# Kernel optimization log

Hardware: AMD Instinct MI355X
Metric: run time of the kernel (lower is better)

## Reference

```python
import jax, jax.numpy as jnp
import numpy as np
from jax import lax

B, T, D_IN, H, L = 512, 256, 2, 100, 3
G = 4 * H  # pytorch gate order: i, f, g, o


def _lstm_layer(xs, W_ih, W_hh, b):
    # xs: [T, B, Din]; W_ih: [4H, Din]; W_hh: [4H, H]; b: [4H] (b_ih + b_hh)
    pre = jnp.einsum('tbd,gd->tbg', xs, W_ih) + b  # [T, B, 4H]

    def step(carry, p):
        h, c = carry
        g = p + h @ W_hh.T
        i, f, gg, o = jnp.split(g, 4, axis=-1)
        c = jax.nn.sigmoid(f) * c + jax.nn.sigmoid(i) * jnp.tanh(gg)
        h = jax.nn.sigmoid(o) * jnp.tanh(c)
        return (h, c), h

    z = jnp.zeros((xs.shape[1], W_hh.shape[1]), xs.dtype)
    _, hs = lax.scan(step, (z, z), pre)
    return hs  # [T, B, H]


def setup_inputs() -> dict:
    key = jax.random.key(0)
    ks = jax.random.split(key, 8)
    s = 1.0 / np.sqrt(H)
    u = lambda k, shp: jax.random.uniform(k, shp, jnp.float32, -s, s)
    return {
        'x': jax.random.normal(ks[0], (B, T, D_IN), jnp.float32),
        'W_ih0': u(ks[1], (G, D_IN)),
        'W_ih_rest': u(ks[2], (L - 1, G, H)),
        'W_hh': u(ks[3], (L, G, H)),
        'b_ih': u(ks[4], (L, G)),
        'b_hh': u(ks[5], (L, G)),
        'head_w': u(ks[6], (1, H)),
        'head_b': u(ks[7], (1,)),
    }


def reference(x, W_ih0, W_ih_rest, W_hh, b_ih, b_hh, head_w, head_b):
    xs = jnp.transpose(x, (1, 0, 2))  # [T, B, D]
    hs = _lstm_layer(xs, W_ih0, W_hh[0], b_ih[0] + b_hh[0])
    for l in range(1, L):  # dropout inactive in eval mode
        hs = _lstm_layer(hs, W_ih_rest[l - 1], W_hh[l], b_ih[l] + b_hh[l])
    last = hs[-1]  # [B, H]
    return last @ head_w.T + head_b  # [B, 1]
```

## Files before the change

### kernel.cpp

```cpp
#include <hip/hip_runtime.h>
#include <math.h>

#define TT 256
#define HH 100
#define GG 400
#define BB 512

typedef float  f32x4  __attribute__((ext_vector_type(4)));
typedef short  bf16x8 __attribute__((ext_vector_type(8)));

#define DPP_ROT1 147
#define DPP_ROT2 78
#define DPP_ROT3 57
#define DPP_XOR1 177
#define DPP_XOR2 78
#define DPP_XOR3 27

template<int CTRL>
__device__ __forceinline__ float dppf(float v) {
    int i = __float_as_int(v);
    int r = __builtin_amdgcn_update_dpp(i, i, CTRL, 0xf, 0xf, false);
    return __int_as_float(r);
}

__device__ __forceinline__ float fexp2(float x) {
    float r; asm("v_exp_f32 %0, %1" : "=v"(r) : "v"(x)); return r;
}
__device__ __forceinline__ float frcp(float x) {
    float r; asm("v_rcp_f32 %0, %1" : "=v"(r) : "v"(x)); return r;
}
#define LOG2E 1.44269504088896f

__device__ __forceinline__ unsigned bf16rne(float x) {
    unsigned b = __float_as_uint(x);
    return (b + 0x7FFFu + ((b >> 16) & 1u)) >> 16;
}

__device__ __forceinline__ void bar_lds() {
    asm volatile("s_waitcnt lgkmcnt(0)" ::: "memory");
    __builtin_amdgcn_s_barrier();
    asm volatile("" ::: "memory");
}

template<int LK>
__global__ void __launch_bounds__(448, 2)
lstm_recur(const float* __restrict__ x,
           const float* __restrict__ pre,
           const float* __restrict__ Whh,
           const float* __restrict__ Wih0,
           const float* __restrict__ bih,
           const float* __restrict__ bhh,
           const float* __restrict__ head_w,
           const float* __restrict__ head_b,
           float* __restrict__ hs,
           float* __restrict__ out)
{
    __shared__ float hbuf[2][4][28];

    const int tid = threadIdx.x;
    const int b   = blockIdx.x;
    const int u   = tid >> 2, ty = tid & 3;
    const int g   = ty * HH + u;
    const bool on = (tid < GG);

    float Wq[4][25];
    float w0a = 0.f, w0b = 0.f, bias = 0.f;
    if (on) {
        #pragma unroll
        for (int d = 0; d < 4; ++d) {
            const float* wrow = Whh + (((ty + d) & 3) * HH + u) * HH + 25 * ty;
            #pragma unroll
            for (int k = 0; k < 25; ++k) Wq[d][k] = wrow[k];
        }
        if (LK == 0) {
            w0a = Wih0[2 * g]; w0b = Wih0[2 * g + 1];
            bias = bih[g] + bhh[g];
        }
    }
    if (tid < 224) (&hbuf[0][0][0])[tid] = 0.f;
    float c = 0.f;
    const int q_w = u / 25, i_w = u % 25;
    __syncthreads();

    float p0 = 0.f;
    float2 xa = {0.f, 0.f};
    if (on) {
        if (LK == 0) xa = *(const float2*)(x + (size_t)b * TT * 2);
        else         p0 = pre[((size_t)0 * BB + b) * GG + g];
    }

    for (int t = 0; t < TT; ++t) {
        const int cur = t & 1, nxt = cur ^ 1;
        if (on) {
            float ext;
            if (LK == 0) ext = bias + w0a * xa.x + w0b * xa.y;
            else         ext = p0;

            const int tn = (t + 1 < TT) ? t + 1 : t;
            if (LK == 0) xa = *(const float2*)(x + ((size_t)b * TT + tn) * 2);
            else         p0 = pre[((size_t)tn * BB + b) * GG + g];

            const float4* hq = (const float4*)&hbuf[cur][ty][0];

            float pA = 0.f, pB = 0.f, pC = 0.f, pD = 0.f;
            #pragma unroll
            for (int i = 0; i < 6; ++i) {
                const float4 h4 = hq[i];
                pA += Wq[0][4*i+0] * h4.x; pB += Wq[1][4*i+0] * h4.x;
                pC += Wq[2][4*i+0] * h4.x; pD += Wq[3][4*i+0] * h4.x;
                pA += Wq[0][4*i+1] * h4.y; pB += Wq[1][4*i+1] * h4.y;
                pC += Wq[2][4*i+1] * h4.y; pD += Wq[3][4*i+1] * h4.y;
                pA += Wq[0][4*i+2] * h4.z; pB += Wq[1][4*i+2] * h4.z;
                pC += Wq[2][4*i+2] * h4.z; pD += Wq[3][4*i+2] * h4.z;
                pA += Wq[0][4*i+3] * h4.w; pB += Wq[1][4*i+3] * h4.w;
                pC += Wq[2][4*i+3] * h4.w; pD += Wq[3][4*i+3] * h4.w;
            }
            const float hl = hq[6].x;
            pA += Wq[0][24] * hl; pB += Wq[1][24] * hl;
            pC += Wq[2][24] * hl; pD += Wq[3][24] * hl;

            float tot = pA + dppf<DPP_ROT1>(pB) + dppf<DPP_ROT2>(pC)
                           + dppf<DPP_ROT3>(pD) + ext;

            const bool isG = (ty == 2);
            float v = isG ? 2.f * tot : tot;
            float s = frcp(1.f + fexp2(-LOG2E * v));
            if (isG) s = 2.f * s - 1.f;

            float B0 = dppf<DPP_XOR1>(s), C0 = dppf<DPP_XOR2>(s), D0 = dppf<DPP_XOR3>(s);

            if (ty == 0) {
                c = B0 * c + s * C0;
                float th = 2.f * frcp(1.f + fexp2(-2.f * LOG2E * c)) - 1.f;
                float hv = D0 * th;
                hbuf[nxt][q_w][i_w] = hv;
                if (LK < 2) hs[((size_t)b * TT + t) * HH + u] = hv;
            }
        }
        bar_lds();
    }

    if (LK == 2 && tid < 64) {
        const int lane = tid;
        float p = hbuf[0][lane / 25][lane % 25] * head_w[lane];
        if (lane < 36) {
            const int k2 = 64 + lane;
            p += hbuf[0][k2 / 25][k2 % 25] * head_w[k2];
        }
        #pragma unroll
        for (int off = 32; off; off >>= 1) p += __shfl_down(p, off);
        if (lane == 0) out[b] = p + head_b[0];
    }
}

__global__ void __launch_bounds__(512, 1)
gemm_pre(const float* __restrict__ hs,
         const float* __restrict__ Wih,
         const float* __restrict__ bih,
         const float* __restrict__ bhh,
         float* __restrict__ pre)
{
    extern __shared__ short Ws[];

    const int tid = threadIdx.x;
    const int l   = tid & 63, w = tid >> 6;
    const int lr  = l & 15, lg = l >> 4;
    const int gbase = blockIdx.y * 200;

    {
        int* wz = (int*)Ws;
        for (int i = tid; i < 26624; i += 512) wz[i] = 0;
    }
    __syncthreads();

    for (int L = tid; L < 20000; L += 512) {
        const int g = L / 100, k = L % 100;
        const float v = Wih[(size_t)(gbase + g) * HH + k];
        const unsigned hh = bf16rne(v);
        const float rem = v - __uint_as_float(hh << 16);
        const unsigned lo = bf16rne(rem);
        const int kp = (((k >> 3) ^ (g & 15)) << 3) | (k & 7);
        Ws[(size_t)g * 128 + kp]          = (short)hh;
        Ws[(size_t)(208 + g) * 128 + kp]  = (short)lo;
    }
    __syncthreads();

    for (int c = 0; c < 8; ++c) {
        const int row0   = blockIdx.x * 1024 + c * 128;
        const int t      = row0 >> 9;
        const int b_base = row0 & 511;

        bf16x8 Ahi[4], Alo[4];
        {
            const float* hrow = hs + ((size_t)(b_base + 16 * w + lr) * TT + t) * HH;
            #pragma unroll
            for (int kt = 0; kt < 4; ++kt) {
                const int k0 = 32 * kt + 8 * lg;
                float4 v0 = {0.f,0.f,0.f,0.f}, v1 = {0.f,0.f,0.f,0.f};
                if (k0     <= 96) v0 = *(const float4*)(hrow + k0);
                if (k0 + 4 <= 96) v1 = *(const float4*)(hrow + k0 + 4);
                const float e[8] = {v0.x,v0.y,v0.z,v0.w,v1.x,v1.y,v1.z,v1.w};
                short sh[8], sl[8];
                #pragma unroll
                for (int i = 0; i < 8; ++i) {
                    const unsigned hh = bf16rne(e[i]);
                    const float rem = e[i] - __uint_as_float(hh << 16);
                    sh[i] = (short)hh;
                    sl[i] = (short)bf16rne(rem);
                }
                Ahi[kt] = (bf16x8){sh[0],sh[1],sh[2],sh[3],sh[4],sh[5],sh[6],sh[7]};
                Alo[kt] = (bf16x8){sl[0],sl[1],sl[2],sl[3],sl[4],sl[5],sl[6],sl[7]};
            }
        }

        #pragma unroll
        for (int n = 0; n < 13; ++n) {
            const int gp = 16 * n + lr;
            bf16x8 Bhi[4], Blo[4];
            #pragma unroll
            for (int kt = 0; kt < 4; ++kt) {
                const int slot = (4 * kt + lg) ^ (gp & 15);
                Bhi[kt] = *(const bf16x8*)&Ws[(size_t)gp * 128 + slot * 8];
                Blo[kt] = *(const bf16x8*)&Ws[(size_t)(208 + gp) * 128 + slot * 8];
            }
            f32x4 acc = {0.f, 0.f, 0.f, 0.f};
            #pragma unroll
            for (int kt = 0; kt < 4; ++kt) {
                acc = __builtin_amdgcn_mfma_f32_16x16x32_bf16(Ahi[kt], Bhi[kt], acc, 0, 0, 0);
                acc = __builtin_amdgcn_mfma_f32_16x16x32_bf16(Alo[kt], Bhi[kt], acc, 0, 0, 0);
                acc = __builtin_amdgcn_mfma_f32_16x16x32_bf16(Ahi[kt], Blo[kt], acc, 0, 0, 0);
            }
            if (gp < 200) {
                const int gcol = gbase + gp;
                const float bsum = bih[gcol] + bhh[gcol];
                #pragma unroll
                for (int r = 0; r < 4; ++r) {
                    const size_t row = (size_t)row0 + 16 * w + 4 * lg + r;
                    pre[row * GG + gcol] = acc[r] + bsum;
                }
            }
        }
    }
}

extern "C" void kernel_launch(void* const* d_in, const int* in_sizes, int n_in,
                              void* d_out, int out_size, void* d_ws, size_t ws_size,
                              hipStream_t stream) {
    const float* x         = (const float*)d_in[0];
    const float* W_ih0     = (const float*)d_in[1];
    const float* W_ih_rest = (const float*)d_in[2];
    const float* W_hh      = (const float*)d_in[3];
    const float* b_ih      = (const float*)d_in[4];
    const float* b_hh      = (const float*)d_in[5];
    const float* head_w    = (const float*)d_in[6];
    const float* head_b    = (const float*)d_in[7];
    float* out = (float*)d_out;

    const size_t HS_BYTES = (size_t)BB * TT * HH * 4;
    float* hs  = (float*)d_ws;
    float* pre = (float*)((char*)d_ws + HS_BYTES);

    const int gemm_lds = 2 * 208 * 128 * 2;
    hipFuncSetAttribute((const void*)gemm_pre,
                        hipFuncAttributeMaxDynamicSharedMemorySize, gemm_lds);
    dim3 ggrid(128, 2);

    lstm_recur<0><<<512, 448, 0, stream>>>(
        x, nullptr, W_hh, W_ih0, b_ih, b_hh, head_w, head_b, hs, out);

    gemm_pre<<<ggrid, 512, gemm_lds, stream>>>(hs, W_ih_rest, b_ih + GG, b_hh + GG, pre);
    lstm_recur<1><<<512, 448, 0, stream>>>(
        nullptr, pre, W_hh + 40000, nullptr, nullptr, nullptr, head_w, head_b, hs, out);

    gemm_pre<<<ggrid, 512, gemm_lds, stream>>>(hs, W_ih_rest + 40000, b_ih + 2*GG, b_hh + 2*GG, pre);
    lstm_recur<2><<<512, 448, 0, stream>>>(
        nullptr, pre, W_hh + 80000, nullptr, nullptr, nullptr, head_w, head_b, hs, out);
}
```

Baseline: 741.3 us.

## Replace layer 1-2 LSTM recurrence with hand-written inline assembly kernel

Adds an inline-assembly recurrence kernel for layers 1 and 2 that keeps the recurrent weights in fixed VGPRs and runs the whole time loop in asm. It uses ds_swizzle for the cross-lane gate reduction and exchange, exp/rcp for the sigmoid and tanh, and prefetches the next step's pre-activation one step ahead. The aim is to cut compiler-generated overhead, waits and instruction count on the serial per-step critical path. It adds fragile hand-allocated registers, explicit exec-mask juggling and heavy VGPR usage that may reduce occupancy under the 448x2 launch bounds.

```diff
diff --git a/kernel.cpp b/kernel.cpp
--- a/kernel.cpp
+++ b/kernel.cpp
@@ -44,16 +44,11 @@
 
 template<int LK>
 __global__ void __launch_bounds__(448, 2)
-lstm_recur(const float* __restrict__ x,
-           const float* __restrict__ pre,
-           const float* __restrict__ Whh,
-           const float* __restrict__ Wih0,
-           const float* __restrict__ bih,
-           const float* __restrict__ bhh,
-           const float* __restrict__ head_w,
-           const float* __restrict__ head_b,
-           float* __restrict__ hs,
-           float* __restrict__ out)
+lstm_recur(const float* __restrict__ x, const float* __restrict__ pre,
+           const float* __restrict__ Whh, const float* __restrict__ Wih0,
+           const float* __restrict__ bih, const float* __restrict__ bhh,
+           const float* __restrict__ head_w, const float* __restrict__ head_b,
+           float* __restrict__ hs, float* __restrict__ out)
 {
     __shared__ float hbuf[2][4][28];
 
@@ -153,11 +148,207 @@
     }
 }
 
+#define FMROW(w0,w1,w2,w3,h) \
+    "v_fmac_f32 v40, v" #w0 ", v" #h "\n\t" \
+    "v_fmac_f32 v41, v" #w1 ", v" #h "\n\t" \
+    "v_fmac_f32 v42, v" #w2 ", v" #h "\n\t" \
+    "v_fmac_f32 v43, v" #w3 ", v" #h "\n\t"
+
+__global__ void __launch_bounds__(448, 2)
+lstm_recur_asm(const float* __restrict__ pre,
+               const float* __restrict__ Whh,
+               const float* __restrict__ head_w,
+               const float* __restrict__ head_b,
+               float* __restrict__ hs,
+               float* __restrict__ out,
+               int do_head)
+{
+    __shared__ __align__(1024) float hbuf[2][4][32];
+
+    const int tid = threadIdx.x;
+    const int b   = blockIdx.x;
+    const int u   = tid >> 2, ty = tid & 3;
+    const int uc  = (u < 100) ? u : 99;
+    const int g   = ty * HH + uc;
+    const bool on = (tid < GG);
+
+    const unsigned long long onm = __ballot(on);
+    const unsigned long long t0m = __ballot(on && ty == 0);
+
+    unsigned wo0 = (unsigned)((((ty ^ 0)) * 100 + uc) * 400 + ty * 100);
+    unsigned wo1 = (unsigned)((((ty ^ 1)) * 100 + uc) * 400 + ty * 100);
+    unsigned wo2 = (unsigned)((((ty ^ 2)) * 100 + uc) * 400 + ty * 100);
+    unsigned wo3 = (unsigned)((((ty ^ 3)) * 100 + uc) * 400 + ty * 100);
+    unsigned pvo    = (unsigned)((b * 400 + g) * 4);
+    unsigned pvomax = pvo + 255u * 819200u;
+    unsigned hso    = (unsigned)(b * 102400 + uc * 4);
+    unsigned hrb = (unsigned)(ty * 128);
+    unsigned hwb = 0x200u + (unsigned)((uc / 25) * 128 + (uc % 25) * 4);
+    float mg = (ty == 2) ? -2.8853900818f : -1.4426950409f;
+    float pk = (ty == 2) ? 2.f : 1.f;
+    float qk = (ty == 2) ? -1.f : 0.f;
+
+    if (tid < 256) (&hbuf[0][0][0])[tid] = 0.f;
+    __syncthreads();
+
+    asm volatile(
+        "s_mov_b64 s[34:35], exec\n\t"
+        "s_mov_b64 exec, %[onm]\n\t"
+        "v_mov_b32 v2, %[wo0]\n\t"
+        "v_mov_b32 v3, %[wo1]\n\t"
+        "v_mov_b32 v4, %[wo2]\n\t"
+        "v_mov_b32 v5, %[wo3]\n\t"
+        "v_mov_b32 v6, %[pvo]\n\t"
+        "v_mov_b32 v7, %[hso]\n\t"
+        "v_mov_b32 v8, %[hrb]\n\t"
+        "v_mov_b32 v9, %[hwb]\n\t"
+        "v_mov_b32 v60, 0\n\t"
+        "global_load_dwordx4 v[100:103], v2, %[whh]\n\t"
+        "global_load_dwordx4 v[104:107], v2, %[whh] offset:16\n\t"
+        "global_load_dwordx4 v[108:111], v2, %[whh] offset:32\n\t"
+        "global_load_dwordx4 v[112:115], v2, %[whh] offset:48\n\t"
+        "global_load_dwordx4 v[116:119], v2, %[whh] offset:64\n\t"
+        "global_load_dwordx4 v[120:123], v2, %[whh] offset:80\n\t"
+        "global_load_dword v124, v2, %[whh] offset:96\n\t"
+        "global_load_dwordx4 v[128:131], v3, %[whh]\n\t"
+        "global_load_dwordx4 v[132:135], v3, %[whh] offset:16\n\t"
+        "global_load_dwordx4 v[136:139], v3, %[whh] offset:32\n\t"
+        "global_load_dwordx4 v[140:143], v3, %[whh] offset:48\n\t"
+        "global_load_dwordx4 v[144:147], v3, %[whh] offset:64\n\t"
+        "global_load_dwordx4 v[148:151], v3, %[whh] offset:80\n\t"
+        "global_load_dword v152, v3, %[whh] offset:96\n\t"
+        "global_load_dwordx4 v[156:159], v4, %[whh]\n\t"
+        "global_load_dwordx4 v[160:163], v4, %[whh] offset:16\n\t"
+        "global_load_dwordx4 v[164:167], v4, %[whh] offset:32\n\t"
+        "global_load_dwordx4 v[168:171], v4, %[whh] offset:48\n\t"
+        "global_load_dwordx4 v[172:175], v4, %[whh] offset:64\n\t"
+        "global_load_dwordx4 v[176:179], v4, %[whh] offset:80\n\t"
+        "global_load_dword v180, v4, %[whh] offset:96\n\t"
+        "global_load_dwordx4 v[184:187], v5, %[whh]\n\t"
+        "global_load_dwordx4 v[188:191], v5, %[whh] offset:16\n\t"
+        "global_load_dwordx4 v[192:195], v5, %[whh] offset:32\n\t"
+        "global_load_dwordx4 v[196:199], v5, %[whh] offset:48\n\t"
+        "global_load_dwordx4 v[200:203], v5, %[whh] offset:64\n\t"
+        "global_load_dwordx4 v[204:207], v5, %[whh] offset:80\n\t"
+        "global_load_dword v208, v5, %[whh] offset:96\n\t"
+        "global_load_dword v10, v6, %[pre]\n\t"
+        "s_movk_i32 s30, 0x100\n\t"
+        "s_waitcnt vmcnt(0)\n\t"
+        "LT%=:\n\t"
+        "s_waitcnt vmcnt(0)\n\t"
+        "v_mov_b32 v11, v10\n\t"
+        "v_add_u32 v6, 0xC8000, v6\n\t"
+        "v_min_u32 v6, v6, %[pvm]\n\t"
+        "global_load_dword v10, v6, %[pre]\n\t"
+        "ds_read_b128 v[12:15], v8\n\t"
+        "ds_read_b128 v[16:19], v8 offset:16\n\t"
+        "ds_read_b128 v[20:23], v8 offset:32\n\t"
+        "ds_read_b128 v[24:27], v8 offset:48\n\t"
+        "ds_read_b128 v[28:31], v8 offset:64\n\t"
+        "ds_read_b128 v[32:35], v8 offset:80\n\t"
+        "ds_read_b128 v[36:39], v8 offset:96\n\t"
+        "v_mov_b32 v40, 0\n\t"
+        "v_mov_b32 v41, 0\n\t"
+        "v_mov_b32 v42, 0\n\t"
+        "v_mov_b32 v43, 0\n\t"
+        "s_waitcnt lgkmcnt(0)\n\t"
+        FMROW(100,128,156,184,12) FMROW(101,129,157,185,13)
+        FMROW(102,130,158,186,14) FMROW(103,131,159,187,15)
+        FMROW(104,132,160,188,16) FMROW(105,133,161,189,17)
+        FMROW(106,134,162,190,18) FMROW(107,135,163,191,19)
+        FMROW(108,136,164,192,20) FMROW(109,137,165,193,21)
+        FMROW(110,138,166,194,22) FMROW(111,139,167,195,23)
+        FMROW(112,140,168,196,24) FMROW(113,141,169,197,25)
+        FMROW(114,142,170,198,26) FMROW(115,143,171,199,27)
+        FMROW(116,144,172,200,28) FMROW(117,145,173,201,29)
+        FMROW(118,146,174,202,30) FMROW(119,147,175,203,31)
+        FMROW(120,148,176,204,32) FMROW(121,149,177,205,33)
+        FMROW(122,150,178,206,34) FMROW(123,151,179,207,35)
+        FMROW(124,152,180,208,36)
+        "ds_swizzle_b32 v44, v41 offset:0x041F\n\t"
+        "ds_swizzle_b32 v45, v42 offset:0x081F\n\t"
+        "ds_swizzle_b32 v46, v43 offset:0x0C1F\n\t"
+        "s_waitcnt lgkmcnt(0)\n\t"
+        "v_add_f32 v40, v40, v44\n\t"
+        "v_add_f32 v40, v40, v45\n\t"
+        "v_add_f32 v40, v40, v46\n\t"
+        "v_add_f32 v40, v40, v11\n\t"
+        "v_mul_f32 v47, %[mg], v40\n\t"
+        "v_exp_f32 v47, v47\n\t"
+        "s_nop 1\n\t"
+        "v_add_f32 v47, 1.0, v47\n\t"
+        "v_rcp_f32 v47, v47\n\t"
+        "s_nop 1\n\t"
+        "v_fma_f32 v44, %[pk], v47, %[qk]\n\t"
+        "ds_swizzle_b32 v45, v44 offset:0x041F\n\t"
+        "ds_swizzle_b32 v46, v44 offset:0x081F\n\t"
+        "ds_swizzle_b32 v48, v44 offset:0x0C1F\n\t"
+        "s_waitcnt lgkmcnt(0)\n\t"
+        "s_mov_b64 exec, %[t0m]\n\t"
+        "v_mul_f32 v60, v45, v60\n\t"
+        "v_fmac_f32 v60, v44, v46\n\t"
+        "v_mul_f32 v49, 0xC038AA3B, v60\n\t"
+        "v_exp_f32 v49, v49\n\t"
+        "s_nop 1\n\t"
+        "v_add_f32 v49, 1.0, v49\n\t"
+        "v_rcp_f32 v49, v49\n\t"
+        "s_nop 1\n\t"
+        "v_fma_f32 v49, 2.0, v49, -1.0\n\t"
+        "v_mul_f32 v50, v48, v49\n\t"
+        "ds_write_b32 v9, v50\n\t"
+        "global_store_dword v7, v50, %[hs]\n\t"
+        "v_add_u32 v7, 0x190, v7\n\t"
+        "s_mov_b64 exec, %[onm]\n\t"
+        "v_xor_b32 v8, 0x200, v8\n\t"
+        "v_xor_b32 v9, 0x200, v9\n\t"
+        "s_waitcnt lgkmcnt(0)\n\t"
+        "s_barrier\n\t"
+        "s_sub_u32 s30, s30, 1\n\t"
+        "s_cmp_lg_u32 s30, 0\n\t"
+        "s_cbranch_scc1 LT%=\n\t"
+        "s_mov_b64 exec, s[34:35]\n\t"
+        :
+        : [onm] "s"(onm), [t0m] "s"(t0m),
+          [whh] "s"(Whh), [pre] "s"(pre), [hs] "s"(hs),
+          [wo0] "v"(wo0), [wo1] "v"(wo1), [wo2] "v"(wo2), [wo3] "v"(wo3),
+          [pvo] "v"(pvo), [pvm] "v"(pvomax), [hso] "v"(hso),
+          [hrb] "v"(hrb), [hwb] "v"(hwb),
+          [mg] "v"(mg), [pk] "v"(pk), [qk] "v"(qk)
+        : "memory", "scc", "s30", "s34", "s35",
+          "v2","v3","v4","v5","v6","v7","v8","v9","v10","v11",
+          "v12","v13","v14","v15","v16","v17","v18","v19","v20","v21",
+          "v22","v23","v24","v25","v26","v27","v28","v29","v30","v31",
+          "v32","v33","v34","v35","v36","v37","v38","v39","v40","v41",
+          "v42","v43","v44","v45","v46","v47","v48","v49","v50","v60",
+          "v100","v101","v102","v103","v104","v105","v106","v107","v108","v109",
+          "v110","v111","v112","v113","v114","v115","v116","v117","v118","v119",
+          "v120","v121","v122","v123","v124","v125","v126","v127","v128","v129",
+          "v130","v131","v132","v133","v134","v135","v136","v137","v138","v139",
+          "v140","v141","v142","v143","v144","v145","v146","v147","v148","v149",
+          "v150","v151","v152","v153","v154","v155","v156","v157","v158","v159",
+          "v160","v161","v162","v163","v164","v165","v166","v167","v168","v169",
+          "v170","v171","v172","v173","v174","v175","v176","v177","v178","v179",
+          "v180","v181","v182","v183","v184","v185","v186","v187","v188","v189",
+          "v190","v191","v192","v193","v194","v195","v196","v197","v198","v199",
+          "v200","v201","v202","v203","v204","v205","v206","v207","v208");
+
+    __syncthreads();
+    if (do_head && tid < 64) {
+        const int lane = tid;
+        float p = hbuf[0][lane / 25][lane % 25] * head_w[lane];
+        if (lane < 36) {
+            const int k2 = 64 + lane;
+            p += hbuf[0][k2 / 25][k2 % 25] * head_w[k2];
+        }
+        #pragma unroll
+        for (int off = 32; off; off >>= 1) p += __shfl_down(p, off);
+        if (lane == 0) out[b] = p + head_b[0];
+    }
+}
+
 __global__ void __launch_bounds__(512, 1)
-gemm_pre(const float* __restrict__ hs,
-         const float* __restrict__ Wih,
-         const float* __restrict__ bih,
-         const float* __restrict__ bhh,
+gemm_pre(const float* __restrict__ hs, const float* __restrict__ Wih,
+         const float* __restrict__ bih, const float* __restrict__ bhh,
          float* __restrict__ pre)
 {
     extern __shared__ short Ws[];
@@ -269,10 +460,10 @@
         x, nullptr, W_hh, W_ih0, b_ih, b_hh, head_w, head_b, hs, out);
 
     gemm_pre<<<ggrid, 512, gemm_lds, stream>>>(hs, W_ih_rest, b_ih + GG, b_hh + GG, pre);
-    lstm_recur<1><<<512, 448, 0, stream>>>(
-        nullptr, pre, W_hh + 40000, nullptr, nullptr, nullptr, head_w, head_b, hs, out);
+    lstm_recur_asm<<<512, 448, 0, stream>>>(
+        pre, W_hh + 40000, head_w, head_b, hs, out, 0);
 
     gemm_pre<<<ggrid, 512, gemm_lds, stream>>>(hs, W_ih_rest + 40000, b_ih + 2*GG, b_hh + 2*GG, pre);
-    lstm_recur<2><<<512, 448, 0, stream>>>(
-        nullptr, pre, W_hh + 80000, nullptr, nullptr, nullptr, head_w, head_b, hs, out);
-}
+    lstm_recur_asm<<<512, 448, 0, stream>>>(
+        pre, W_hh + 80000, head_w, head_b, hs, out, 1);
+}
```

After: 925.3 us. 1.25x slower.

## Replace layers 1-2 recurrence with hand-written asm kernel processing two batches per block

Applied to the files above, without the earlier changes.

Adds an inline-assembly LSTM recurrence kernel for layers 1 and 2. Each 1024-thread block handles two batch rows, so every W_hh register load serves two sequences. Each gate row is split across 8 lanes, partial sums are reduced with ds_swizzle, and the next step's pre-activation is prefetched. This targets per-step latency and weight-register reuse in the serial time loop. The cost is fragile hard-coded register allocation, exec-mask handling and barrier ordering, with half as many blocks in flight.

```diff
diff --git a/kernel.cpp b/kernel.cpp
--- a/kernel.cpp
+++ b/kernel.cpp
@@ -44,16 +44,11 @@
 
 template<int LK>
 __global__ void __launch_bounds__(448, 2)
-lstm_recur(const float* __restrict__ x,
-           const float* __restrict__ pre,
-           const float* __restrict__ Whh,
-           const float* __restrict__ Wih0,
-           const float* __restrict__ bih,
-           const float* __restrict__ bhh,
-           const float* __restrict__ head_w,
-           const float* __restrict__ head_b,
-           float* __restrict__ hs,
-           float* __restrict__ out)
+lstm_recur(const float* __restrict__ x, const float* __restrict__ pre,
+           const float* __restrict__ Whh, const float* __restrict__ Wih0,
+           const float* __restrict__ bih, const float* __restrict__ bhh,
+           const float* __restrict__ head_w, const float* __restrict__ head_b,
+           float* __restrict__ hs, float* __restrict__ out)
 {
     __shared__ float hbuf[2][4][28];
 
@@ -153,11 +148,295 @@
     }
 }
 
+#define FME(wa,wb,wc,wd,h0,h1) \
+    "v_fmac_f32 v44, v" #wa ", v" #h0 "\n\t" \
+    "v_fmac_f32 v45, v" #wb ", v" #h0 "\n\t" \
+    "v_fmac_f32 v46, v" #wc ", v" #h0 "\n\t" \
+    "v_fmac_f32 v47, v" #wd ", v" #h0 "\n\t" \
+    "v_fmac_f32 v48, v" #wa ", v" #h1 "\n\t" \
+    "v_fmac_f32 v49, v" #wb ", v" #h1 "\n\t" \
+    "v_fmac_f32 v50, v" #wc ", v" #h1 "\n\t" \
+    "v_fmac_f32 v51, v" #wd ", v" #h1 "\n\t"
+
+__global__ void __launch_bounds__(1024, 1)
+lstm_recur_asm(const float* __restrict__ pre,
+               const float* __restrict__ Whh,
+               const float* __restrict__ head_w,
+               const float* __restrict__ head_b,
+               float* __restrict__ hs,
+               float* __restrict__ out,
+               int do_head)
+{
+    __shared__ __align__(2048) float hbuf[2][256];
+
+    const int tid = threadIdx.x;
+    const int b0  = blockIdx.x * 2;
+    const int u   = tid >> 3;
+    const int s   = tid & 7;
+    const int ty  = s >> 1;
+    const int uc  = (u < 100) ? u : 99;
+    const int g   = ty * HH + uc;
+    const bool on = (u < 100);
+
+    const unsigned long long onm = __ballot(on);
+    const unsigned long long m7  = onm & ~__ballot(s == 7);
+    const unsigned long long wrm = __ballot(on && s == 0);
+
+    unsigned wo0 = (unsigned)((((ty ^ 0)) * 100 + uc) * 400 + s * 52);
+    unsigned wo1 = (unsigned)((((ty ^ 1)) * 100 + uc) * 400 + s * 52);
+    unsigned wo2 = (unsigned)((((ty ^ 2)) * 100 + uc) * 400 + s * 52);
+    unsigned wo3 = (unsigned)((((ty ^ 3)) * 100 + uc) * 400 + s * 52);
+    unsigned pv0  = (unsigned)((b0    ) * 1600 + g * 4);
+    unsigned pv1  = (unsigned)((b0 + 1) * 1600 + g * 4);
+    unsigned pvm0 = pv0 + 255u * 819200u;
+    unsigned pvm1 = pv1 + 255u * 819200u;
+    unsigned hs0  = (unsigned)(b0 * 102400 + uc * 4);
+    unsigned hrb  = (unsigned)(s * 52);
+    unsigned hwb  = 0x400u + (unsigned)(uc * 4);
+    float mg = (ty == 2) ? -2.8853900818f : -1.4426950409f;
+    float pk = (ty == 2) ? 2.f : 1.f;
+    float qk = (ty == 2) ? -1.f : 0.f;
+
+    if (tid < 512) (&hbuf[0][0])[tid] = 0.f;
+    __syncthreads();
+
+    asm volatile(
+        "s_mov_b64 s[34:35], exec\n\t"
+        "s_mov_b64 exec, %[onm]\n\t"
+        "v_mov_b32 v2, %[wo0]\n\t"
+        "v_mov_b32 v3, %[wo1]\n\t"
+        "v_mov_b32 v4, %[wo2]\n\t"
+        "v_mov_b32 v5, %[wo3]\n\t"
+        "v_mov_b32 v6, %[pv0]\n\t"
+        "v_mov_b32 v7, %[pv1]\n\t"
+        "v_mov_b32 v8, %[hrb]\n\t"
+        "v_mov_b32 v9, %[hwb]\n\t"
+        "v_mov_b32 v10, %[hs0]\n\t"
+        "v_add_u32 v11, 0x19000, v10\n\t"
+        "v_mov_b32 v61, 0\n\t"
+        "v_mov_b32 v62, 0\n\t"
+        "v_mov_b32 v73, 0\n\t"  "v_mov_b32 v74, 0\n\t"
+        "v_mov_b32 v75, 0\n\t"  "v_mov_b32 v76, 0\n\t"
+        "v_mov_b32 v86, 0\n\t"  "v_mov_b32 v87, 0\n\t"
+        "v_mov_b32 v88, 0\n\t"  "v_mov_b32 v89, 0\n\t"
+        "v_mov_b32 v99, 0\n\t"  "v_mov_b32 v100, 0\n\t"
+        "v_mov_b32 v101, 0\n\t" "v_mov_b32 v102, 0\n\t"
+        "v_mov_b32 v112, 0\n\t" "v_mov_b32 v113, 0\n\t"
+        "v_mov_b32 v114, 0\n\t" "v_mov_b32 v115, 0\n\t"
+        "global_load_dword v64, v2, %[whh]\n\t"
+        "global_load_dword v65, v2, %[whh] offset:4\n\t"
+        "global_load_dword v66, v2, %[whh] offset:8\n\t"
+        "global_load_dword v67, v2, %[whh] offset:12\n\t"
+        "global_load_dword v68, v2, %[whh] offset:16\n\t"
+        "global_load_dword v69, v2, %[whh] offset:20\n\t"
+        "global_load_dword v70, v2, %[whh] offset:24\n\t"
+        "global_load_dword v71, v2, %[whh] offset:28\n\t"
+        "global_load_dword v72, v2, %[whh] offset:32\n\t"
+        "global_load_dword v77, v3, %[whh]\n\t"
+        "global_load_dword v78, v3, %[whh] offset:4\n\t"
+        "global_load_dword v79, v3, %[whh] offset:8\n\t"
+        "global_load_dword v80, v3, %[whh] offset:12\n\t"
+        "global_load_dword v81, v3, %[whh] offset:16\n\t"
+        "global_load_dword v82, v3, %[whh] offset:20\n\t"
+        "global_load_dword v83, v3, %[whh] offset:24\n\t"
+        "global_load_dword v84, v3, %[whh] offset:28\n\t"
+        "global_load_dword v85, v3, %[whh] offset:32\n\t"
+        "global_load_dword v90, v4, %[whh]\n\t"
+        "global_load_dword v91, v4, %[whh] offset:4\n\t"
+        "global_load_dword v92, v4, %[whh] offset:8\n\t"
+        "global_load_dword v93, v4, %[whh] offset:12\n\t"
+        "global_load_dword v94, v4, %[whh] offset:16\n\t"
+        "global_load_dword v95, v4, %[whh] offset:20\n\t"
+        "global_load_dword v96, v4, %[whh] offset:24\n\t"
+        "global_load_dword v97, v4, %[whh] offset:28\n\t"
+        "global_load_dword v98, v4, %[whh] offset:32\n\t"
+        "global_load_dword v103, v5, %[whh]\n\t"
+        "global_load_dword v104, v5, %[whh] offset:4\n\t"
+        "global_load_dword v105, v5, %[whh] offset:8\n\t"
+        "global_load_dword v106, v5, %[whh] offset:12\n\t"
+        "global_load_dword v107, v5, %[whh] offset:16\n\t"
+        "global_load_dword v108, v5, %[whh] offset:20\n\t"
+        "global_load_dword v109, v5, %[whh] offset:24\n\t"
+        "global_load_dword v110, v5, %[whh] offset:28\n\t"
+        "global_load_dword v111, v5, %[whh] offset:32\n\t"
+        "s_mov_b64 exec, %[m7]\n\t"
+        "global_load_dword v73, v2, %[whh] offset:36\n\t"
+        "global_load_dword v74, v2, %[whh] offset:40\n\t"
+        "global_load_dword v75, v2, %[whh] offset:44\n\t"
+        "global_load_dword v76, v2, %[whh] offset:48\n\t"
+        "global_load_dword v86, v3, %[whh] offset:36\n\t"
+        "global_load_dword v87, v3, %[whh] offset:40\n\t"
+        "global_load_dword v88, v3, %[whh] offset:44\n\t"
+        "global_load_dword v89, v3, %[whh] offset:48\n\t"
+        "global_load_dword v99, v4, %[whh] offset:36\n\t"
+        "global_load_dword v100, v4, %[whh] offset:40\n\t"
+        "global_load_dword v101, v4, %[whh] offset:44\n\t"
+        "global_load_dword v102, v4, %[whh] offset:48\n\t"
+        "global_load_dword v112, v5, %[whh] offset:36\n\t"
+        "global_load_dword v113, v5, %[whh] offset:40\n\t"
+        "global_load_dword v114, v5, %[whh] offset:44\n\t"
+        "global_load_dword v115, v5, %[whh] offset:48\n\t"
+        "s_mov_b64 exec, %[onm]\n\t"
+        "global_load_dword v12, v6, %[pre]\n\t"
+        "global_load_dword v13, v7, %[pre]\n\t"
+        "s_movk_i32 s30, 0x100\n\t"
+        "s_waitcnt vmcnt(0)\n\t"
+        "LT%=:\n\t"
+        "s_waitcnt vmcnt(0)\n\t"
+        "v_mov_b32 v14, v12\n\t"
+        "v_mov_b32 v15, v13\n\t"
+        "v_add_u32 v6, 0xC8000, v6\n\t"
+        "v_min_u32 v6, v6, %[pvm0]\n\t"
+        "v_add_u32 v7, 0xC8000, v7\n\t"
+        "v_min_u32 v7, v7, %[pvm1]\n\t"
+        "global_load_dword v12, v6, %[pre]\n\t"
+        "global_load_dword v13, v7, %[pre]\n\t"
+        "ds_read2_b32 v[16:17], v8 offset0:0 offset1:1\n\t"
+        "ds_read2_b32 v[18:19], v8 offset0:2 offset1:3\n\t"
+        "ds_read2_b32 v[20:21], v8 offset0:4 offset1:5\n\t"
+        "ds_read2_b32 v[22:23], v8 offset0:6 offset1:7\n\t"
+        "ds_read2_b32 v[24:25], v8 offset0:8 offset1:9\n\t"
+        "ds_read2_b32 v[26:27], v8 offset0:10 offset1:11\n\t"
+        "ds_read_b32 v28, v8 offset:48\n\t"
+        "ds_read2_b32 v[30:31], v8 offset0:128 offset1:129\n\t"
+        "ds_read2_b32 v[32:33], v8 offset0:130 offset1:131\n\t"
+        "ds_read2_b32 v[34:35], v8 offset0:132 offset1:133\n\t"
+        "ds_read2_b32 v[36:37], v8 offset0:134 offset1:135\n\t"
+        "ds_read2_b32 v[38:39], v8 offset0:136 offset1:137\n\t"
+        "ds_read2_b32 v[40:41], v8 offset0:138 offset1:139\n\t"
+        "ds_read_b32 v42, v8 offset:560\n\t"
+        "v_mov_b32 v44, 0\n\t" "v_mov_b32 v45, 0\n\t"
+        "v_mov_b32 v46, 0\n\t" "v_mov_b32 v47, 0\n\t"
+        "v_mov_b32 v48, 0\n\t" "v_mov_b32 v49, 0\n\t"
+        "v_mov_b32 v50, 0\n\t" "v_mov_b32 v51, 0\n\t"
+        "s_waitcnt lgkmcnt(0)\n\t"
+        FME(64,77,90,103,16,30)   FME(65,78,91,104,17,31)
+        FME(66,79,92,105,18,32)   FME(67,80,93,106,19,33)
+        FME(68,81,94,107,20,34)   FME(69,82,95,108,21,35)
+        FME(70,83,96,109,22,36)   FME(71,84,97,110,23,37)
+        FME(72,85,98,111,24,38)   FME(73,86,99,112,25,39)
+        FME(74,87,100,113,26,40)  FME(75,88,101,114,27,41)
+        FME(76,89,102,115,28,42)
+        "ds_swizzle_b32 v52, v44 offset:0x041F\n\t"
+        "ds_swizzle_b32 v53, v45 offset:0x041F\n\t"
+        "ds_swizzle_b32 v54, v46 offset:0x041F\n\t"
+        "ds_swizzle_b32 v55, v47 offset:0x041F\n\t"
+        "ds_swizzle_b32 v56, v48 offset:0x041F\n\t"
+        "ds_swizzle_b32 v57, v49 offset:0x041F\n\t"
+        "ds_swizzle_b32 v58, v50 offset:0x041F\n\t"
+        "ds_swizzle_b32 v59, v51 offset:0x041F\n\t"
+        "s_waitcnt lgkmcnt(0)\n\t"
+        "v_add_f32 v44, v44, v52\n\t"
+        "v_add_f32 v45, v45, v53\n\t"
+        "v_add_f32 v46, v46, v54\n\t"
+        "v_add_f32 v47, v47, v55\n\t"
+        "v_add_f32 v48, v48, v56\n\t"
+        "v_add_f32 v49, v49, v57\n\t"
+        "v_add_f32 v50, v50, v58\n\t"
+        "v_add_f32 v51, v51, v59\n\t"
+        "ds_swizzle_b32 v52, v45 offset:0x081F\n\t"
+        "ds_swizzle_b32 v53, v46 offset:0x101F\n\t"
+        "ds_swizzle_b32 v54, v47 offset:0x181F\n\t"
+        "ds_swizzle_b32 v56, v49 offset:0x081F\n\t"
+        "ds_swizzle_b32 v57, v50 offset:0x101F\n\t"
+        "ds_swizzle_b32 v58, v51 offset:0x181F\n\t"
+        "s_waitcnt lgkmcnt(0)\n\t"
+        "v_add_f32 v55, v44, v52\n\t"
+        "v_add_f32 v55, v55, v53\n\t"
+        "v_add_f32 v55, v55, v54\n\t"
+        "v_add_f32 v55, v55, v14\n\t"
+        "v_add_f32 v59, v48, v56\n\t"
+        "v_add_f32 v59, v59, v57\n\t"
+        "v_add_f32 v59, v59, v58\n\t"
+        "v_add_f32 v59, v59, v15\n\t"
+        "v_mul_f32 v52, %[mg], v55\n\t"
+        "v_exp_f32 v52, v52\n\t"
+        "v_mul_f32 v53, %[mg], v59\n\t"
+        "v_exp_f32 v53, v53\n\t"
+        "s_nop 1\n\t"
+        "v_add_f32 v52, 1.0, v52\n\t"
+        "v_add_f32 v53, 1.0, v53\n\t"
+        "v_rcp_f32 v52, v52\n\t"
+        "v_rcp_f32 v53, v53\n\t"
+        "s_nop 1\n\t"
+        "v_fma_f32 v57, %[pk], v52, %[qk]\n\t"
+        "v_fma_f32 v58, %[pk], v53, %[qk]\n\t"
+        "ds_swizzle_b32 v52, v57 offset:0x081F\n\t"
+        "ds_swizzle_b32 v53, v57 offset:0x101F\n\t"
+        "ds_swizzle_b32 v54, v57 offset:0x181F\n\t"
+        "ds_swizzle_b32 v44, v58 offset:0x081F\n\t"
+        "ds_swizzle_b32 v45, v58 offset:0x101F\n\t"
+        "ds_swizzle_b32 v46, v58 offset:0x181F\n\t"
+        "s_waitcnt lgkmcnt(0)\n\t"
+        "s_mov_b64 exec, %[wrm]\n\t"
+        "v_mul_f32 v61, v52, v61\n\t"
+        "v_fmac_f32 v61, v57, v53\n\t"
+        "v_mul_f32 v62, v44, v62\n\t"
+        "v_fmac_f32 v62, v58, v45\n\t"
+        "v_mul_f32 v55, 0xC038AA3B, v61\n\t"
+        "v_exp_f32 v55, v55\n\t"
+        "v_mul_f32 v59, 0xC038AA3B, v62\n\t"
+        "v_exp_f32 v59, v59\n\t"
+        "s_nop 1\n\t"
+        "v_add_f32 v55, 1.0, v55\n\t"
+        "v_add_f32 v59, 1.0, v59\n\t"
+        "v_rcp_f32 v55, v55\n\t"
+        "v_rcp_f32 v59, v59\n\t"
+        "s_nop 1\n\t"
+        "v_fma_f32 v55, 2.0, v55, -1.0\n\t"
+        "v_fma_f32 v59, 2.0, v59, -1.0\n\t"
+        "v_mul_f32 v55, v54, v55\n\t"
+        "v_mul_f32 v59, v46, v59\n\t"
+        "ds_write_b32 v9, v55\n\t"
+        "ds_write_b32 v9, v59 offset:512\n\t"
+        "global_store_dword v10, v55, %[hs]\n\t"
+        "global_store_dword v11, v59, %[hs]\n\t"
+        "v_add_u32 v10, 0x190, v10\n\t"
+        "v_add_u32 v11, 0x190, v11\n\t"
+        "s_mov_b64 exec, %[onm]\n\t"
+        "v_xor_b32 v8, 0x400, v8\n\t"
+        "v_xor_b32 v9, 0x400, v9\n\t"
+        "s_waitcnt lgkmcnt(0)\n\t"
+        "s_barrier\n\t"
+        "s_sub_u32 s30, s30, 1\n\t"
+        "s_cmp_lg_u32 s30, 0\n\t"
+        "s_cbranch_scc1 LT%=\n\t"
+        "s_mov_b64 exec, s[34:35]\n\t"
+        :
+        : [onm] "s"(onm), [m7] "s"(m7), [wrm] "s"(wrm),
+          [whh] "s"(Whh), [pre] "s"(pre), [hs] "s"(hs),
+          [wo0] "v"(wo0), [wo1] "v"(wo1), [wo2] "v"(wo2), [wo3] "v"(wo3),
+          [pv0] "v"(pv0), [pv1] "v"(pv1), [pvm0] "v"(pvm0), [pvm1] "v"(pvm1),
+          [hs0] "v"(hs0), [hrb] "v"(hrb), [hwb] "v"(hwb),
+          [mg] "v"(mg), [pk] "v"(pk), [qk] "v"(qk)
+        : "memory", "scc", "s30", "s34", "s35",
+          "v2","v3","v4","v5","v6","v7","v8","v9","v10","v11",
+          "v12","v13","v14","v15","v16","v17","v18","v19","v20","v21",
+          "v22","v23","v24","v25","v26","v27","v28","v29","v30","v31",
+          "v32","v33","v34","v35","v36","v37","v38","v39","v40","v41",
+          "v42","v43","v44","v45","v46","v47","v48","v49","v50","v51",
+          "v52","v53","v54","v55","v56","v57","v58","v59","v60","v61","v62",
+          "v64","v65","v66","v67","v68","v69","v70","v71","v72","v73",
+          "v74","v75","v76","v77","v78","v79","v80","v81","v82","v83",
+          "v84","v85","v86","v87","v88","v89","v90","v91","v92","v93",
+          "v94","v95","v96","v97","v98","v99","v100","v101","v102","v103",
+          "v104","v105","v106","v107","v108","v109","v110","v111","v112",
+          "v113","v114","v115");
+
+    __syncthreads();
+    if (do_head && tid < 128) {
+        const int lane = tid & 63, wv = tid >> 6;
+        float p = hbuf[0][wv * 128 + lane] * head_w[lane];
+        if (lane < 36) p += hbuf[0][wv * 128 + 64 + lane] * head_w[64 + lane];
+        #pragma unroll
+        for (int off = 32; off; off >>= 1) p += __shfl_down(p, off);
+        if (lane == 0) out[b0 + wv] = p + head_b[0];
+    }
+}
+
 __global__ void __launch_bounds__(512, 1)
-gemm_pre(const float* __restrict__ hs,
-         const float* __restrict__ Wih,
-         const float* __restrict__ bih,
-         const float* __restrict__ bhh,
+gemm_pre(const float* __restrict__ hs, const float* __restrict__ Wih,
+         const float* __restrict__ bih, const float* __restrict__ bhh,
          float* __restrict__ pre)
 {
     extern __shared__ short Ws[];
@@ -269,10 +548,10 @@
         x, nullptr, W_hh, W_ih0, b_ih, b_hh, head_w, head_b, hs, out);
 
     gemm_pre<<<ggrid, 512, gemm_lds, stream>>>(hs, W_ih_rest, b_ih + GG, b_hh + GG, pre);
-    lstm_recur<1><<<512, 448, 0, stream>>>(
-        nullptr, pre, W_hh + 40000, nullptr, nullptr, nullptr, head_w, head_b, hs, out);
+    lstm_recur_asm<<<256, 1024, 0, stream>>>(
+        pre, W_hh + 40000, head_w, head_b, hs, out, 0);
 
     gemm_pre<<<ggrid, 512, gemm_lds, stream>>>(hs, W_ih_rest + 40000, b_ih + 2*GG, b_hh + 2*GG, pre);
-    lstm_recur<2><<<512, 448, 0, stream>>>(
-        nullptr, pre, W_hh + 80000, nullptr, nullptr, nullptr, head_w, head_b, hs, out);
-}
+    lstm_recur_asm<<<256, 1024, 0, stream>>>(
+        pre, W_hh + 80000, head_w, head_b, hs, out, 1);
+}
```

Result: slower. 939.3 us (+26.7%).
